# Kernel tuning notes

Hardware: AMD Instinct MI355X
Metric: run time of the kernel (lower is better)

## Reference

```python
import jax, jax.numpy as jnp
import numpy as np

B, S, D, H = 2, 2048, 1024, 16
DK = D // H

def setup_inputs() -> dict:
    key = jax.random.key(0)
    ks = jax.random.split(key, 12)
    sc = 0.02
    return {
        "q": jax.random.normal(ks[0], (B, S, D), jnp.float32),
        "k": jax.random.normal(ks[1], (B, S, D), jnp.float32),
        "v": jax.random.normal(ks[2], (B, S, D), jnp.float32),
        "mask": jnp.ones((1, 1, S, S), jnp.int32),
        "w_q": jax.random.normal(ks[3], (D, D), jnp.float32) * sc,
        "b_q": jnp.zeros((D,), jnp.float32),
        "w_k": jax.random.normal(ks[4], (D, D), jnp.float32) * sc,
        "b_k": jnp.zeros((D,), jnp.float32),
        "w_v": jax.random.normal(ks[5], (D, D), jnp.float32) * sc,
        "b_v": jnp.zeros((D,), jnp.float32),
        "w_o": jax.random.normal(ks[6], (D, D), jnp.float32) * sc,
        "b_o": jnp.zeros((D,), jnp.float32),
    }

def reference(q, k, v, mask, w_q, b_q, w_k, b_k, w_v, b_v, w_o, b_o):
    # torch Linear: y = x @ W.T + b, W is [out, in]
    def lin(x, w, b):
        return jnp.einsum('bsd,ed->bse', x, w) + b
    # project and split heads -> [B, H, S, DK]
    def heads(x):
        return x.reshape(B, S, H, DK).transpose(0, 2, 1, 3)
    Q = heads(lin(q, w_q, b_q))
    K = heads(lin(k, w_k, b_k))
    V = heads(lin(v, w_v, b_v))
    scores = jnp.einsum('bhqd,bhkd->bhqk', Q, K) / jnp.sqrt(jnp.float32(DK))
    scores = jnp.where(mask == 0, jnp.float32(-1e9), scores)
    attn = jax.nn.softmax(scores, axis=-1)  # dropout p=0 -> identity
    ctx = jnp.einsum('bhqk,bhkd->bhqd', attn, V)
    ctx = ctx.transpose(0, 2, 1, 3).reshape(B, S, D)
    return lin(ctx, w_o, b_o)
```

## Files before the change

kernel.cpp:

```cpp
#include <hip/hip_runtime.h>
#include <stdint.h>


#define S_LEN 2048
#define LOG2E 1.4426950408889634f

using bf16x8 = __attribute__((ext_vector_type(8))) __bf16;
using f32x4 = __attribute__((ext_vector_type(4))) float;
using f32x16 = __attribute__((ext_vector_type(16))) float;
using u32x4 = __attribute__((ext_vector_type(4))) unsigned int;

__device__ __forceinline__ unsigned short f2bf(float x) {
  unsigned int u = __builtin_bit_cast(unsigned int, x);
  u += 0x7fffu + ((u >> 16) & 1u);
  return (unsigned short)(u >> 16);
}

__device__ __forceinline__ void gload_lds16(const void* g, void* l) {
  __builtin_amdgcn_global_load_lds(
      (const __attribute__((address_space(1))) void*)g,
      (__attribute__((address_space(3))) void*)l, 16, 0, 0);
}

__device__ __forceinline__ unsigned int cvtpk(float lo, float hi) {
  unsigned int r;
  asm("v_cvt_pk_bf16_f32 %0, %1, %2" : "=v"(r) : "v"(lo), "v"(hi));
  return r;
}

__device__ __forceinline__ bf16x8 mkfrag(float p0, float p1, float p2, float p3,
                                         float p4, float p5, float p6, float p7) {
  auto r02 = __builtin_amdgcn_permlane32_swap(cvtpk(p0, p1), cvtpk(p4, p5),
                                              false, false);
  auto r13 = __builtin_amdgcn_permlane32_swap(cvtpk(p2, p3), cvtpk(p6, p7),
                                              false, false);
  u32x4 w = {(unsigned int)r02[0], (unsigned int)r13[0], (unsigned int)r02[1],
             (unsigned int)r13[1]};
  return __builtin_bit_cast(bf16x8, w);
}

__global__ void cvt7_kernel(const float* __restrict__ q,
                            const float* __restrict__ k,
                            const float* __restrict__ v,
                            const float* __restrict__ w0,
                            const float* __restrict__ w1,
                            const float* __restrict__ w2,
                            const float* __restrict__ w3,
                            unsigned short* __restrict__ dq,
                            unsigned short* __restrict__ dk,
                            unsigned short* __restrict__ dv,
                            unsigned short* __restrict__ e0,
                            unsigned short* __restrict__ e1,
                            unsigned short* __restrict__ e2,
                            unsigned short* __restrict__ e3) {
  const int y = blockIdx.y;
  const float* src;
  unsigned short* dst;
  int n4;
  if (y < 3) {
    src = y == 0 ? q : y == 1 ? k : v;
    dst = y == 0 ? dq : y == 1 ? dk : dv;
    n4 = 1048576;
  } else {
    int j = y - 3;
    src = j == 0 ? w0 : j == 1 ? w1 : j == 2 ? w2 : w3;
    dst = j == 0 ? e0 : j == 1 ? e1 : j == 2 ? e2 : e3;
    n4 = 262144;
  }
  int i = blockIdx.x * blockDim.x + threadIdx.x;
  int stride = gridDim.x * blockDim.x;
  for (; i < n4; i += stride) {
    float4 a = ((const float4*)src)[i];
    ushort4 o;
    o.x = f2bf(a.x);
    o.y = f2bf(a.y);
    o.z = f2bf(a.z);
    o.w = f2bf(a.w);
    ((ushort4*)dst)[i] = o;
  }
}

template <int OMODE>
__device__ __forceinline__ void qkv128_body(
    unsigned short* As, unsigned short* Bs,
    const unsigned short* __restrict__ X, const unsigned short* __restrict__ W,
    const float* __restrict__ bias, unsigned short* __restrict__ dst,
    float scale, int tx, int ty) {
  const int tid = threadIdx.x;
  const int wid = tid >> 6, lane = tid & 63;
  const int l15 = lane & 15, lg = lane >> 4;
  const int bm = ty * 128, bn = tx * 128;
  const int wr = (wid >> 1) * 64, wc = (wid & 1) * 64;

  const f32x4 fz = {0.f, 0.f, 0.f, 0.f};
  f32x4 acc[4][4];
#pragma unroll
  for (int m = 0; m < 4; ++m)
#pragma unroll
    for (int n = 0; n < 4; ++n) acc[m][n] = fz;

  const int srow = lane >> 3;
  const int sslot = (lane & 7) ^ srow;
  const int l7 = l15 & 7;

  for (int kt = 0; kt < 1024; kt += 64) {
#pragma unroll
    for (int c = 0; c < 4; ++c) {
      int ch = wid * 4 + c;
      gload_lds16(X + (size_t)(bm + ch * 8 + srow) * 1024 + kt + sslot * 8,
                  As + ch * 512);
      gload_lds16(W + (size_t)(bn + ch * 8 + srow) * 1024 + kt + sslot * 8,
                  Bs + ch * 512);
    }
    __syncthreads();

#pragma unroll
    for (int kc = 0; kc < 2; ++kc) {
      const int rcol = ((kc * 4 + lg) ^ l7) * 8;
      bf16x8 af[4], bf[4];
#pragma unroll
      for (int m = 0; m < 4; ++m)
        af[m] = *(const bf16x8*)&As[(wr + m * 16 + l15) * 64 + rcol];
#pragma unroll
      for (int n = 0; n < 4; ++n)
        bf[n] = *(const bf16x8*)&Bs[(wc + n * 16 + l15) * 64 + rcol];

#pragma unroll
      for (int m = 0; m < 4; ++m)
#pragma unroll
        for (int n = 0; n < 4; ++n) {
          if (OMODE == 2)
            acc[m][n] = __builtin_amdgcn_mfma_f32_16x16x32_bf16(
                bf[n], af[m], acc[m][n], 0, 0, 0);
          else
            acc[m][n] = __builtin_amdgcn_mfma_f32_16x16x32_bf16(
                af[m], bf[n], acc[m][n], 0, 0, 0);
        }
    }
    __syncthreads();
  }

#pragma unroll
  for (int m = 0; m < 4; ++m)
#pragma unroll
    for (int n = 0; n < 4; ++n)
#pragma unroll
      for (int j = 0; j < 4; ++j) {
        float a = acc[m][n][j];
        if (OMODE == 2) {
          int gn = bn + wc + n * 16 + lg * 4 + j;
          int gm = bm + wr + m * 16 + l15;
          float v = a + bias[gn];
          int b = gm >> 11, s = gm & 2047;
          int h = gn >> 6, dk = gn & 63;
          dst[(((size_t)(b * 16 + h)) * 64 + dk) * 2048 + s] = f2bf(v);
        } else {
          int gm = bm + wr + m * 16 + lg * 4 + j;
          int gn = bn + wc + n * 16 + l15;
          float v = (a + bias[gn]) * scale;
          int b = gm >> 11, s = gm & 2047;
          int h = gn >> 6, dk = gn & 63;
          dst[(((size_t)(b * 16 + h)) * 2048 + s) * 64 + dk] = f2bf(v);
        }
      }
}

__global__ __launch_bounds__(256) void gemm_qkv(
    const unsigned short* __restrict__ X0, const unsigned short* __restrict__ X1,
    const unsigned short* __restrict__ X2, const unsigned short* __restrict__ W0,
    const unsigned short* __restrict__ W1,
    const unsigned short* __restrict__ W2, const float* __restrict__ b0,
    const float* __restrict__ b1, const float* __restrict__ b2,
    unsigned short* __restrict__ dq, unsigned short* __restrict__ dk,
    unsigned short* __restrict__ dv) {
  __shared__ unsigned short As[128 * 64];
  __shared__ unsigned short Bs[128 * 64];
  const int lin = blockIdx.x + 8 * (blockIdx.y + 32 * blockIdx.z);
  const int xcd = lin & 7, v = lin >> 3;
  const int panel = xcd * 12 + (v >> 3);
  const int tx = v & 7;
  const int z = panel >> 5, ty = panel & 31;
  if (z == 0)
    qkv128_body<0>(As, Bs, X0, W0, b0, dq, 0.125f * LOG2E, tx, ty);
  else if (z == 1)
    qkv128_body<0>(As, Bs, X1, W1, b1, dk, 1.0f, tx, ty);
  else
    qkv128_body<2>(As, Bs, X2, W2, b2, dv, 1.0f, tx, ty);
}

__global__ __launch_bounds__(256) void gemm_out(
    const unsigned short* __restrict__ X, const unsigned short* __restrict__ W,
    const float* __restrict__ bias, float* __restrict__ dstF) {
  const int lin = blockIdx.x + 8 * blockIdx.y;
  const int xcd = lin & 7, v = lin >> 3;
  const int ty = xcd * 8 + (v >> 3);
  const int tx = v & 7;

  __shared__ unsigned short As[3][64 * 32];
  __shared__ unsigned short Bs[3][128 * 32];
  const int tid = threadIdx.x;
  const int wid = tid >> 6, lane = tid & 63;
  const int l15 = lane & 15, lg = lane >> 4;
  const int bm = ty * 64, bn = tx * 128;
  const int wr = (wid >> 1) * 32, wc = (wid & 1) * 64;

  const f32x4 fz = {0.f, 0.f, 0.f, 0.f};
  f32x4 acc[2][4];
#pragma unroll
  for (int m = 0; m < 2; ++m)
#pragma unroll
    for (int n = 0; n < 4; ++n) acc[m][n] = fz;

  const int srow = lane >> 2;
  const int scolz = ((lane & 3) ^ ((lane >> 3) & 3)) * 8;
  const int rcol = (lg ^ ((l15 >> 1) & 3)) * 8;

#define GSTAGE(buf, kt)                                                       \
  {                                                                           \
    gload_lds16(X + (size_t)(bm + wid * 16 + srow) * 1024 + (kt) + scolz,     \
                &As[buf][wid * 512]);                                         \
    _Pragma("unroll") for (int c = 0; c < 2; ++c) {                           \
      int ch = wid * 2 + c;                                                   \
      gload_lds16(W + (size_t)(bn + ch * 16 + srow) * 1024 + (kt) + scolz,    \
                  &Bs[buf][ch * 512]);                                        \
    }                                                                         \
  }

  GSTAGE(0, 0)
  GSTAGE(1, 32)
  int cur = 0;

  for (int it = 0; it < 32; ++it) {
    if (it < 31) {
      asm volatile("s_waitcnt vmcnt(3)\n\ts_barrier" ::: "memory");
    } else {
      asm volatile("s_waitcnt vmcnt(0)\n\ts_barrier" ::: "memory");
    }
    if (it < 30) {
      int nb = cur >= 1 ? cur - 1 : cur + 2;
      GSTAGE(nb, (it + 2) * 32)
    }

    bf16x8 af[2], bf[4];
#pragma unroll
    for (int m = 0; m < 2; ++m)
      af[m] = *(const bf16x8*)&As[cur][(wr + m * 16 + l15) * 32 + rcol];
#pragma unroll
    for (int n = 0; n < 4; ++n)
      bf[n] = *(const bf16x8*)&Bs[cur][(wc + n * 16 + l15) * 32 + rcol];

#pragma unroll
    for (int m = 0; m < 2; ++m)
#pragma unroll
      for (int n = 0; n < 4; ++n)
        acc[m][n] = __builtin_amdgcn_mfma_f32_16x16x32_bf16(af[m], bf[n],
                                                            acc[m][n], 0, 0, 0);
    cur = cur == 2 ? 0 : cur + 1;
  }
#undef GSTAGE

#pragma unroll
  for (int m = 0; m < 2; ++m)
#pragma unroll
    for (int n = 0; n < 4; ++n)
#pragma unroll
      for (int j = 0; j < 4; ++j) {
        int gm = bm + wr + m * 16 + lg * 4 + j;
        int gn = bn + wc + n * 16 + l15;
        dstF[(size_t)gm * 1024 + gn] = acc[m][n][j] + bias[gn];
      }
}

__global__ __launch_bounds__(256) void attn_kernel(
    const unsigned short* __restrict__ Q,
    const unsigned short* __restrict__ K,
    const unsigned short* __restrict__ VT,
    unsigned short* __restrict__ CTX) {
  const int orig = blockIdx.x;
  const int idx = (orig & 7) * 64 + (orig >> 3);
  const int bh = idx >> 4;
  const int qb = idx & 15;
  const int tid = threadIdx.x;
  const int w = tid >> 6;
  const int lane = tid & 63;
  const int l31 = lane & 31;
  const int hi = lane >> 5;
  const int q0 = qb * 128 + w * 32;

  __shared__ __align__(16) unsigned short Ks[2][64][64];
  __shared__ __align__(16) unsigned short Vs[2][64][64];

  const unsigned short* Qg = Q + ((size_t)bh * S_LEN + q0) * 64;
  const unsigned short* Kg = K + (size_t)bh * S_LEN * 64;
  const unsigned short* Vg = VT + (size_t)bh * 64 * S_LEN;

  bf16x8 qf[4];
#pragma unroll
  for (int kc = 0; kc < 4; ++kc)
    qf[kc] = *(const bf16x8*)&Qg[l31 * 64 + kc * 16 + hi * 8];

  const u32x4 ow = {0x3F803F80u, 0x3F803F80u, 0x3F803F80u, 0x3F803F80u};
  const bf16x8 onesf = __builtin_bit_cast(bf16x8, ow);

  const int srow = lane >> 3;
  const int sslot = (lane & 7) ^ srow;

#define STAGE_K(buf, kt)                                                      \
  {                                                                           \
    gload_lds16(Kg + ((size_t)((kt) + w * 16 + srow)) * 64 + sslot * 8,       \
                &Ks[buf][w * 16][0]);                                         \
    gload_lds16(Kg + ((size_t)((kt) + w * 16 + 8 + srow)) * 64 + sslot * 8,   \
                &Ks[buf][w * 16 + 8][0]);                                     \
  }
#define STAGE_V(buf, kt)                                                       \
  {                                                                            \
    gload_lds16(Vg + ((size_t)(w * 16 + srow)) * S_LEN + (kt) + sslot * 8,     \
                &Vs[buf][w * 16][0]);                                          \
    gload_lds16(Vg + ((size_t)(w * 16 + 8 + srow)) * S_LEN + (kt) + sslot * 8, \
                &Vs[buf][w * 16 + 8][0]);                                      \
  }

  const f32x16 fz16 = {};
  f32x16 O0 = {}, O1 = {}, Lacc = {};
  f32x16 sA0, sA1, sB0, sB1;

  STAGE_K(0, 0)
  STAGE_V(0, 0)
  STAGE_K(1, 64)
  asm volatile("s_waitcnt vmcnt(2)\n\ts_barrier" ::: "memory");
  sA0 = fz16;
  sA1 = fz16;
  __builtin_amdgcn_s_setprio(1);
#pragma unroll
  for (int kc = 0; kc < 4; ++kc) {
    const int col = ((kc * 2 + hi) ^ (l31 & 7)) * 8;
    bf16x8 kf0 = *(const bf16x8*)&Ks[0][l31][col];
    bf16x8 kf1 = *(const bf16x8*)&Ks[0][32 + l31][col];
    sA0 = __builtin_amdgcn_mfma_f32_32x32x16_bf16(kf0, qf[kc], sA0, 0, 0, 0);
    sA1 = __builtin_amdgcn_mfma_f32_32x32x16_bf16(kf1, qf[kc], sA1, 0, 0, 0);
  }
  __builtin_amdgcn_s_setprio(0);
  STAGE_V(1, 64)

#define BODY(T, SP0, SP1, SN0, SN1, PB, DO_PRE, DO_QK)                         \
  {                                                                            \
    if (DO_QK) {                                                               \
      asm volatile("s_waitcnt vmcnt(2)\n\ts_barrier" ::: "memory");            \
    } else {                                                                   \
      asm volatile("s_waitcnt vmcnt(0)\n\ts_barrier" ::: "memory");            \
    }                                                                          \
    if (DO_PRE) STAGE_K(PB, ((T) + 2) * 64)                                    \
    if (DO_QK) {                                                               \
      SN0 = fz16;                                                              \
      SN1 = fz16;                                                              \
      __builtin_amdgcn_s_setprio(1);                                           \
      _Pragma("unroll") for (int kc = 0; kc < 4; ++kc) {                       \
        const int col = ((kc * 2 + hi) ^ (l31 & 7)) * 8;                       \
        bf16x8 kf0 = *(const bf16x8*)&Ks[1 - (PB)][l31][col];                  \
        bf16x8 kf1 = *(const bf16x8*)&Ks[1 - (PB)][32 + l31][col];             \
        SN0 =                                                                  \
            __builtin_amdgcn_mfma_f32_32x32x16_bf16(kf0, qf[kc], SN0, 0, 0, 0);\
        SN1 =                                                                  \
            __builtin_amdgcn_mfma_f32_32x32x16_bf16(kf1, qf[kc], SN1, 0, 0, 0);\
      }                                                                        \
      __builtin_amdgcn_s_setprio(0);                                           \
    }                                                                          \
    _Pragma("unroll") for (int r = 0; r < 16; ++r) {                           \
      SP0[r] = exp2f(SP0[r]);                                                  \
      SP1[r] = exp2f(SP1[r]);                                                  \
    }                                                                          \
    {                                                                          \
      bf16x8 pa0 = mkfrag(SP0[0], SP0[1], SP0[2], SP0[3], SP0[4], SP0[5],      \
                          SP0[6], SP0[7]);                                     \
      bf16x8 pa1 = mkfrag(SP0[8], SP0[9], SP0[10], SP0[11], SP0[12], SP0[13],  \
                          SP0[14], SP0[15]);                                   \
      bf16x8 pa2 = mkfrag(SP1[0], SP1[1], SP1[2], SP1[3], SP1[4], SP1[5],      \
                          SP1[6], SP1[7]);                                     \
      bf16x8 pa3 = mkfrag(SP1[8], SP1[9], SP1[10], SP1[11], SP1[12], SP1[13],  \
                          SP1[14], SP1[15]);                                   \
      __builtin_amdgcn_s_setprio(1);                                           \
      _Pragma("unroll") for (int kc = 0; kc < 4; ++kc) {                       \
        const int col = ((kc * 2 + hi) ^ (l31 & 7)) * 8;                       \
        bf16x8 v0 = *(const bf16x8*)&Vs[PB][l31][col];                         \
        bf16x8 v1 = *(const bf16x8*)&Vs[PB][32 + l31][col];                    \
        bf16x8 pa = (kc == 0) ? pa0 : (kc == 1) ? pa1 : (kc == 2) ? pa2 : pa3; \
        O0 = __builtin_amdgcn_mfma_f32_32x32x16_bf16(pa, v0, O0, 0, 0, 0);     \
        O1 = __builtin_amdgcn_mfma_f32_32x32x16_bf16(pa, v1, O1, 0, 0, 0);     \
        Lacc = __builtin_amdgcn_mfma_f32_32x32x16_bf16(pa, onesf, Lacc, 0, 0,  \
                                                       0);                     \
      }                                                                        \
      __builtin_amdgcn_s_setprio(0);                                           \
    }                                                                          \
    asm volatile("s_barrier" ::: "memory");                                    \
    if (DO_PRE) STAGE_V(PB, ((T) + 2) * 64)                                    \
  }

  for (int tt = 0; tt < 15; ++tt) {
    const int te = 2 * tt;
    BODY(te, sA0, sA1, sB0, sB1, 0, 1, 1)
    BODY(te + 1, sB0, sB1, sA0, sA1, 1, 1, 1)
  }
  BODY(30, sA0, sA1, sB0, sB1, 0, 0, 1)
  BODY(31, sB0, sB1, sA0, sA1, 1, 0, 0)
#undef BODY
#undef STAGE_K
#undef STAGE_V

  const int b = bh >> 4, h = bh & 15;
#pragma unroll
  for (int r = 0; r < 16; ++r) {
    int qr = (r & 3) + 8 * (r >> 2) + 4 * hi;
    float inv = __builtin_amdgcn_rcpf(Lacc[r]);
    size_t base = ((size_t)b * S_LEN + q0 + qr) * 1024 + h * 64;
    CTX[base + l31] = f2bf(O0[r] * inv);
    CTX[base + 32 + l31] = f2bf(O1[r] * inv);
  }
}

extern "C" void kernel_launch(void* const* d_in, const int* in_sizes, int n_in,
                              void* d_out, int out_size, void* d_ws,
                              size_t ws_size, hipStream_t stream) {
  const float* q = (const float*)d_in[0];
  const float* k = (const float*)d_in[1];
  const float* v = (const float*)d_in[2];
  const float* wq = (const float*)d_in[4];
  const float* bq = (const float*)d_in[5];
  const float* wk = (const float*)d_in[6];
  const float* bk = (const float*)d_in[7];
  const float* wv = (const float*)d_in[8];
  const float* bv = (const float*)d_in[9];
  const float* wo = (const float*)d_in[10];
  const float* bo = (const float*)d_in[11];
  float* out = (float*)d_out;

  const size_t NTOK = 4096 * 1024;
  unsigned short* ws = (unsigned short*)d_ws;
  unsigned short* xq = ws;
  unsigned short* xk = xq + NTOK;
  unsigned short* xv = xk + NTOK;
  unsigned short* wqb = xv + NTOK;
  unsigned short* wkb = wqb + 1048576;
  unsigned short* wvb = wkb + 1048576;
  unsigned short* wob = wvb + 1048576;
  unsigned short* Qp = wob + 1048576;
  unsigned short* Kp = Qp + NTOK;
  unsigned short* Vt = Kp + NTOK;
  unsigned short* CTX = ws;

  cvt7_kernel<<<dim3(512, 7), 256, 0, stream>>>(q, k, v, wq, wk, wv, wo, xq, xk,
                                                xv, wqb, wkb, wvb, wob);

  gemm_qkv<<<dim3(8, 32, 3), 256, 0, stream>>>(xq, xk, xv, wqb, wkb, wvb, bq,
                                               bk, bv, Qp, Kp, Vt);

  attn_kernel<<<512, 256, 0, stream>>>(Qp, Kp, Vt, CTX);

  gemm_out<<<dim3(8, 64), 256, 0, stream>>>(CTX, wob, bo, out);
}
```

Measured before the change: 138.7 us.

## Replace triple-buffered out-projection GEMM with single-buffer 64-wide K tiles

Rewrites the output projection GEMM to load 64-wide K tiles into one shared buffer, with a barrier before and after compute, instead of a three-stage async prefetch pipeline over 32-wide tiles. This halves the loop iterations and uses an 8-way XOR swizzle for the wider rows. In exchange, global loads no longer overlap with MFMA work, so memory latency is exposed on each iteration.

New measurement: 133.8 us. 1.04x faster.

```diff
diff --git a/kernel.cpp b/kernel.cpp
--- a/kernel.cpp
+++ b/kernel.cpp
@@ -191,13 +191,13 @@
 __global__ __launch_bounds__(256) void gemm_out(
     const unsigned short* __restrict__ X, const unsigned short* __restrict__ W,
     const float* __restrict__ bias, float* __restrict__ dstF) {
+  __shared__ unsigned short As[64 * 64];
+  __shared__ unsigned short Bs[128 * 64];
   const int lin = blockIdx.x + 8 * blockIdx.y;
   const int xcd = lin & 7, v = lin >> 3;
   const int ty = xcd * 8 + (v >> 3);
   const int tx = v & 7;
 
-  __shared__ unsigned short As[3][64 * 32];
-  __shared__ unsigned short Bs[3][128 * 32];
   const int tid = threadIdx.x;
   const int wid = tid >> 6, lane = tid & 63;
   const int l15 = lane & 15, lg = lane >> 4;
@@ -211,53 +211,45 @@
 #pragma unroll
     for (int n = 0; n < 4; ++n) acc[m][n] = fz;
 
-  const int srow = lane >> 2;
-  const int scolz = ((lane & 3) ^ ((lane >> 3) & 3)) * 8;
-  const int rcol = (lg ^ ((l15 >> 1) & 3)) * 8;
-
-#define GSTAGE(buf, kt)                                                       \
-  {                                                                           \
-    gload_lds16(X + (size_t)(bm + wid * 16 + srow) * 1024 + (kt) + scolz,     \
-                &As[buf][wid * 512]);                                         \
-    _Pragma("unroll") for (int c = 0; c < 2; ++c) {                           \
-      int ch = wid * 2 + c;                                                   \
-      gload_lds16(W + (size_t)(bn + ch * 16 + srow) * 1024 + (kt) + scolz,    \
-                  &Bs[buf][ch * 512]);                                        \
-    }                                                                         \
-  }
-
-  GSTAGE(0, 0)
-  GSTAGE(1, 32)
-  int cur = 0;
-
-  for (int it = 0; it < 32; ++it) {
-    if (it < 31) {
-      asm volatile("s_waitcnt vmcnt(3)\n\ts_barrier" ::: "memory");
-    } else {
-      asm volatile("s_waitcnt vmcnt(0)\n\ts_barrier" ::: "memory");
+  const int srow = lane >> 3;
+  const int sslot = (lane & 7) ^ srow;
+  const int l7 = l15 & 7;
+
+  for (int kt = 0; kt < 1024; kt += 64) {
+#pragma unroll
+    for (int c = 0; c < 2; ++c) {
+      int ch = wid * 2 + c;
+      gload_lds16(X + (size_t)(bm + ch * 8 + srow) * 1024 + kt + sslot * 8,
+                  As + ch * 512);
     }
-    if (it < 30) {
-      int nb = cur >= 1 ? cur - 1 : cur + 2;
-      GSTAGE(nb, (it + 2) * 32)
+#pragma unroll
+    for (int c = 0; c < 4; ++c) {
+      int ch = wid * 4 + c;
+      gload_lds16(W + (size_t)(bn + ch * 8 + srow) * 1024 + kt + sslot * 8,
+                  Bs + ch * 512);
     }
-
-    bf16x8 af[2], bf[4];
-#pragma unroll
-    for (int m = 0; m < 2; ++m)
-      af[m] = *(const bf16x8*)&As[cur][(wr + m * 16 + l15) * 32 + rcol];
-#pragma unroll
-    for (int n = 0; n < 4; ++n)
-      bf[n] = *(const bf16x8*)&Bs[cur][(wc + n * 16 + l15) * 32 + rcol];
-
-#pragma unroll
-    for (int m = 0; m < 2; ++m)
+    __syncthreads();
+
+#pragma unroll
+    for (int kc = 0; kc < 2; ++kc) {
+      const int rcol = ((kc * 4 + lg) ^ l7) * 8;
+      bf16x8 af[2], bf[4];
+#pragma unroll
+      for (int m = 0; m < 2; ++m)
+        af[m] = *(const bf16x8*)&As[(wr + m * 16 + l15) * 64 + rcol];
 #pragma unroll
       for (int n = 0; n < 4; ++n)
-        acc[m][n] = __builtin_amdgcn_mfma_f32_16x16x32_bf16(af[m], bf[n],
-                                                            acc[m][n], 0, 0, 0);
-    cur = cur == 2 ? 0 : cur + 1;
-  }
-#undef GSTAGE
+        bf[n] = *(const bf16x8*)&Bs[(wc + n * 16 + l15) * 64 + rcol];
+
+#pragma unroll
+      for (int m = 0; m < 2; ++m)
+#pragma unroll
+        for (int n = 0; n < 4; ++n)
+          acc[m][n] = __builtin_amdgcn_mfma_f32_16x16x32_bf16(
+              af[m], bf[n], acc[m][n], 0, 0, 0);
+    }
+    __syncthreads();
+  }
 
 #pragma unroll
   for (int m = 0; m < 2; ++m)
```
